# Optimization experiments

Hardware: AMD Instinct MI355X
Metric: run time of the kernel (lower is better)

Reference implementation:

```python
import jax, jax.numpy as jnp
import numpy as np
import math


def setup_inputs() -> dict:
    key = jax.random.key(0)
    kq, kk, kv, km = jax.random.split(key, 4)
    B, Lq, Lk, D = 4, 4096, 4096, 64
    queries = jax.random.normal(kq, (B, Lq, D), dtype=jnp.float32)
    keys = jax.random.normal(kk, (B, Lk, D), dtype=jnp.float32)
    values = jax.random.normal(kv, (B, Lk, D), dtype=jnp.float32)
    masks = jax.random.randint(km, (B, Lk), 0, 2, dtype=jnp.int32)
    return {"queries": queries, "keys": keys, "values": values, "masks": masks}


def reference(queries, keys, values, masks):
    # scale = sqrt(d_k) (self.scale is None)
    d_k = queries.shape[-1]
    scale = math.sqrt(d_k)
    # scores: [B, Lq, Lk]
    scores = jnp.einsum('bqd,bkd->bqk', queries, keys) / jnp.asarray(scale, queries.dtype)
    # key-padding mask [B, Lk] -> broadcast over Lq; masked positions -> -inf
    neg_inf = jnp.asarray(float('-inf'), scores.dtype)
    scores = jnp.where(masks[:, None, :] == 0, neg_inf, scores)
    attn = jax.nn.softmax(scores, axis=-1)  # dropout p=0 -> identity
    return jnp.einsum('bqk,bkd->bqd', attn, values)
```

## Files before the change

kernel.cpp:

```cpp
#include <hip/hip_runtime.h>


#define B_N    4
#define L      4096
#define DH     64
#define TILE_K 64
#define KPAD   72
#define SPLIT  8
#define SLAB   (L / SPLIT)
#define TILES  (SLAB / TILE_K)
#define QSCALE 0.18033688f

typedef unsigned short ushort8_ma __attribute__((ext_vector_type(8), may_alias));
typedef unsigned short ushort4_ma __attribute__((ext_vector_type(4), may_alias));
typedef float          f32x4_ma   __attribute__((ext_vector_type(4), may_alias));
typedef short          short8     __attribute__((ext_vector_type(8)));
typedef float          f32x16     __attribute__((ext_vector_type(16)));

union v8cast { ushort8_ma u; short8 s; };

static __device__ __forceinline__ short8 ld8(const unsigned short* p) {
    v8cast x; x.u = *(const ushort8_ma*)p; return x.s;
}
static __device__ __forceinline__ unsigned short bf16rne(float f) {
    union { float f; unsigned u; } x; x.f = f;
    unsigned r = x.u + 0x7fffu + ((x.u >> 16) & 1u);
    return (unsigned short)(r >> 16);
}
static __device__ __forceinline__ unsigned short bf16fast(float f) {
    union { float f; unsigned u; } x; x.f = f;
    return (unsigned short)((x.u + 0x8000u) >> 16);
}
static __device__ __forceinline__ float bf16tof(unsigned short u) {
    union { unsigned u; float f; } x; x.u = (unsigned)u << 16; return x.f;
}
static __device__ __forceinline__ float fast_exp2(float x) {
    return __builtin_amdgcn_exp2f(x);
}

__global__ __launch_bounds__(256)
void prepass3(const float* __restrict__ Q, const float* __restrict__ K,
              const float* __restrict__ V,
              unsigned short* __restrict__ Qb, unsigned short* __restrict__ Kb,
              unsigned short* __restrict__ Vt)
{
    __shared__ unsigned short t[64][20];
    const int b  = blockIdx.y;
    const int r0 = blockIdx.x * 16;
    const size_t base = ((size_t)b * L + r0) * DH;

    {
        int i = threadIdx.x;
        int row = i >> 4, d0 = (i & 15) * 4;
        size_t off = base + (size_t)row * DH + d0;
        f32x4_ma q = *(const f32x4_ma*)(Q + off);
        f32x4_ma k = *(const f32x4_ma*)(K + off);
        f32x4_ma v = *(const f32x4_ma*)(V + off);
        ushort4_ma qo, ko;
        #pragma unroll
        for (int j = 0; j < 4; ++j) {
            qo[j] = bf16rne(q[j] * QSCALE);
            ko[j] = bf16rne(k[j]);
            t[d0 + j][row] = bf16rne(v[j]);
        }
        *(ushort4_ma*)(Qb + off) = qo;
        *(ushort4_ma*)(Kb + off) = ko;
    }
    __syncthreads();
    {
        int i = threadIdx.x;
        int d = i >> 2, k4 = (i & 3) * 4;
        ushort4_ma vo = { t[d][k4], t[d][k4 + 1], t[d][k4 + 2], t[d][k4 + 3] };
        *(ushort4_ma*)(Vt + ((size_t)b * DH + d) * L + r0 + k4) = vo;
    }
}

__global__ __launch_bounds__(256, 4)
void fa_split32(const unsigned short* __restrict__ Qb,
                const unsigned short* __restrict__ Kb,
                const unsigned short* __restrict__ Vt,
                const int*            __restrict__ Mk,
                unsigned short* __restrict__ ACCp, float* __restrict__ Lp)
{
    __shared__ unsigned short Kl[TILE_K * KPAD];
    __shared__ unsigned short Vl[DH * KPAD];
    __shared__ unsigned short Pl[4][32 * KPAD];
    __shared__ int            Ml[TILE_K];

    const int tid  = threadIdx.x;
    const int wave = tid >> 6;
    const int lane = tid & 63;
    const int l32  = lane & 31;
    const int hw   = lane >> 5;

    const int b      = blockIdx.y & (B_N - 1);
    const int slab   = blockIdx.y >> 2;
    const int qblock = blockIdx.x * 128;
    const int kbase  = slab * SLAB;

    short8 aQ[4];
    {
        const unsigned short* qp = Qb + ((size_t)b * L + qblock + wave * 32 + l32) * DH;
        #pragma unroll
        for (int kk = 0; kk < 4; ++kk)
            aQ[kk] = ld8(qp + kk * 16 + hw * 8);
    }

    const unsigned short* Kbb = Kb + (size_t)b * L * DH;
    const unsigned short* Vtb = Vt + (size_t)b * DH * L;
    const int*            Mb  = Mk + (size_t)b * L;

    const int c1 = tid + 256;
    const int r0 = tid >> 3, d0 = (tid & 7) * 8;
    const int r1 = c1 >> 3,  d1 = (c1 & 7) * 8;

    ushort8_ma kr0, kr1, vr0, vr1;
    int mr;

    kr0 = *(const ushort8_ma*)(Kbb + (size_t)(kbase + r0) * DH + d0);
    kr1 = *(const ushort8_ma*)(Kbb + (size_t)(kbase + r1) * DH + d1);
    vr0 = *(const ushort8_ma*)(Vtb + (size_t)r0 * L + kbase + d0);
    vr1 = *(const ushort8_ma*)(Vtb + (size_t)r1 * L + kbase + d1);
    mr  = Mb[kbase + lane];
    *(ushort8_ma*)(&Kl[r0 * KPAD + d0]) = kr0;
    *(ushort8_ma*)(&Kl[r1 * KPAD + d1]) = kr1;
    *(ushort8_ma*)(&Vl[r0 * KPAD + d0]) = vr0;
    *(ushort8_ma*)(&Vl[r1 * KPAD + d1]) = vr1;
    if (wave == 0) Ml[lane] = mr;
    __syncthreads();

    f32x16 acc0 = {0}, acc1 = {0};
    float rs[16];
    #pragma unroll
    for (int r = 0; r < 16; ++r) rs[r] = 0.f;

    unsigned short* pw = &Pl[wave][0];

    for (int t = 0; t < TILES; ++t) {
        if (t < TILES - 1) {
            const int k0n = kbase + (t + 1) * TILE_K;
            kr0 = *(const ushort8_ma*)(Kbb + (size_t)(k0n + r0) * DH + d0);
            kr1 = *(const ushort8_ma*)(Kbb + (size_t)(k0n + r1) * DH + d1);
            vr0 = *(const ushort8_ma*)(Vtb + (size_t)r0 * L + k0n + d0);
            vr1 = *(const ushort8_ma*)(Vtb + (size_t)r1 * L + k0n + d1);
            mr  = Mb[k0n + lane];
        }

        #pragma unroll
        for (int g = 0; g < 2; ++g) {
            f32x16 s = {0};
            #pragma unroll
            for (int kk = 0; kk < 4; ++kk) {
                short8 bK = ld8(&Kl[(g * 32 + l32) * KPAD + kk * 16 + hw * 8]);
                s = __builtin_amdgcn_mfma_f32_32x32x16_bf16(aQ[kk], bK, s, 0, 0, 0);
            }
            float bias = (Ml[g * 32 + l32] == 0) ? -1e30f : 0.f;
            #pragma unroll
            for (int reg = 0; reg < 16; ++reg) {
                float p = fast_exp2(s[reg] + bias);
                rs[reg] += p;
                int row = (reg & 3) + 8 * (reg >> 2) + 4 * hw;
                pw[row * KPAD + g * 32 + l32] = bf16fast(p);
            }
        }

        #pragma unroll
        for (int kk = 0; kk < 4; ++kk) {
            short8 aP = ld8(&pw[l32 * KPAD + kk * 16 + hw * 8]);
            short8 bV0 = ld8(&Vl[l32 * KPAD + kk * 16 + hw * 8]);
            acc0 = __builtin_amdgcn_mfma_f32_32x32x16_bf16(aP, bV0, acc0, 0, 0, 0);
            short8 bV1 = ld8(&Vl[(32 + l32) * KPAD + kk * 16 + hw * 8]);
            acc1 = __builtin_amdgcn_mfma_f32_32x32x16_bf16(aP, bV1, acc1, 0, 0, 0);
        }

        __syncthreads();
        if (t < TILES - 1) {
            *(ushort8_ma*)(&Kl[r0 * KPAD + d0]) = kr0;
            *(ushort8_ma*)(&Kl[r1 * KPAD + d1]) = kr1;
            *(ushort8_ma*)(&Vl[r0 * KPAD + d0]) = vr0;
            *(ushort8_ma*)(&Vl[r1 * KPAD + d1]) = vr1;
            if (wave == 0) Ml[lane] = mr;
            __syncthreads();
        }
    }

    const size_t pbase = ((size_t)(slab * B_N + b)) * L;
    #pragma unroll
    for (int reg = 0; reg < 16; ++reg) {
        float t0 = rs[reg];
        t0 += __shfl_xor(t0, 1);
        t0 += __shfl_xor(t0, 2);
        t0 += __shfl_xor(t0, 4);
        t0 += __shfl_xor(t0, 8);
        t0 += __shfl_xor(t0, 16);
        int row  = (reg & 3) + 8 * (reg >> 2) + 4 * hw;
        int qrow = qblock + wave * 32 + row;
        unsigned short* ap = ACCp + (pbase + qrow) * DH;
        ap[l32]      = bf16rne(acc0[reg]);
        ap[32 + l32] = bf16rne(acc1[reg]);
        if (l32 == 0) Lp[pbase + qrow] = t0;
    }
}

__global__ __launch_bounds__(256)
void fa_combine(const unsigned short* __restrict__ ACCp,
                const float* __restrict__ Lp, float* __restrict__ O)
{
    const int b    = blockIdx.y;
    const int qrow = blockIdx.x * 4 + (threadIdx.x >> 6);
    const int d    = threadIdx.x & 63;

    float lsum = 0.f, o = 0.f;
    #pragma unroll
    for (int s = 0; s < SPLIT; ++s) {
        lsum += Lp[((size_t)(s * B_N + b)) * L + qrow];
        o    += bf16tof(ACCp[(((size_t)(s * B_N + b)) * L + qrow) * DH + d]);
    }
    O[((size_t)b * L + qrow) * DH + d] = o / fmaxf(lsum, 1e-20f);
}

#define TK  64
#define RW  4
#define RB  16
#define KST 67

__global__ __launch_bounds__(256)
void fa_scalar(const float* __restrict__ Q, const float* __restrict__ K,
               const float* __restrict__ V, const int* __restrict__ Mk,
               float* __restrict__ O)
{
    __shared__ float Kt[TK][KST];
    __shared__ float Vts[DH][KST];
    __shared__ float Qs[RB][DH];
    __shared__ float Ps[4][RW][TK];
    __shared__ float Bs[TK];

    const int tid = threadIdx.x, w = tid >> 6, lane = tid & 63;
    const int b = blockIdx.y, row0 = blockIdx.x * RB;

    for (int i = tid; i < RB * DH; i += 256) {
        int r = i >> 6, d = i & 63;
        Qs[r][d] = Q[((size_t)b * L + row0 + r) * DH + d];
    }
    float m[RW], l[RW], acc[RW];
    #pragma unroll
    for (int rr = 0; rr < RW; ++rr) { m[rr] = -1e30f; l[rr] = 0.f; acc[rr] = 0.f; }

    for (int k0 = 0; k0 < L; k0 += TK) {
        __syncthreads();
        for (int i = tid; i < TK * DH; i += 256) {
            int key = i >> 6, d = i & 63;
            Kt[key][d]  = K[((size_t)b * L + k0 + key) * DH + d];
            Vts[d][key] = V[((size_t)b * L + k0 + key) * DH + d];
        }
        if (tid < TK) Bs[tid] = (Mk[(size_t)b * L + k0 + tid] == 0) ? -1e30f : 0.f;
        __syncthreads();
        float s[RW];
        #pragma unroll
        for (int rr = 0; rr < RW; ++rr) s[rr] = 0.f;
        for (int d4 = 0; d4 < DH; d4 += 4) {
            float kv[4];
            #pragma unroll
            for (int j = 0; j < 4; ++j) kv[j] = Kt[lane][d4 + j];
            #pragma unroll
            for (int rr = 0; rr < RW; ++rr)
                #pragma unroll
                for (int j = 0; j < 4; ++j)
                    s[rr] += Qs[w * RW + rr][d4 + j] * kv[j];
        }
        float alpha[RW];
        #pragma unroll
        for (int rr = 0; rr < RW; ++rr) {
            float sv = s[rr] * 0.125f + Bs[lane];
            float t = sv;
            #pragma unroll
            for (int off = 1; off < 64; off <<= 1) t = fmaxf(t, __shfl_xor(t, off));
            float mnew = fmaxf(m[rr], t);
            alpha[rr] = __expf(fminf(m[rr] - mnew, 0.f));
            float p = __expf(fminf(sv - mnew, 0.f));
            Ps[w][rr][lane] = p;
            float su = p;
            #pragma unroll
            for (int off = 1; off < 64; off <<= 1) su += __shfl_xor(su, off);
            l[rr] = l[rr] * alpha[rr] + su;
            m[rr] = mnew;
        }
        __syncthreads();
        #pragma unroll
        for (int rr = 0; rr < RW; ++rr) acc[rr] *= alpha[rr];
        for (int k4 = 0; k4 < TK; k4 += 4) {
            float vv[4];
            #pragma unroll
            for (int j = 0; j < 4; ++j) vv[j] = Vts[lane][k4 + j];
            #pragma unroll
            for (int rr = 0; rr < RW; ++rr)
                #pragma unroll
                for (int j = 0; j < 4; ++j)
                    acc[rr] += Ps[w][rr][k4 + j] * vv[j];
        }
    }
    #pragma unroll
    for (int rr = 0; rr < RW; ++rr) {
        int row = row0 + w * RW + rr;
        O[((size_t)b * L + row) * DH + lane] = acc[rr] / fmaxf(l[rr], 1e-20f);
    }
}

extern "C" void kernel_launch(void* const* d_in, const int* in_sizes, int n_in,
                              void* d_out, int out_size, void* d_ws, size_t ws_size,
                              hipStream_t stream) {
    const float* Q = (const float*)d_in[0];
    const float* K = (const float*)d_in[1];
    const float* V = (const float*)d_in[2];
    const int*   M = (const int*)d_in[3];
    float*       O = (float*)d_out;

    const size_t elems     = (size_t)B_N * L * DH;
    const size_t bf16_need = elems * 2 * 3;
    const size_t acc_elems = (size_t)SPLIT * B_N * L * DH;
    const size_t ml_elems  = (size_t)SPLIT * B_N * L;
    const size_t full_need = bf16_need + acc_elems * 2 + ml_elems * 4;

    unsigned short* Qb = (unsigned short*)d_ws;
    unsigned short* Kb = Qb + elems;
    unsigned short* Vt = Kb + elems;

    if (ws_size >= full_need) {
        unsigned short* ACCp = Vt + elems;
        float*          Lp   = (float*)(ACCp + acc_elems);

        prepass3<<<dim3(L / 16, B_N), dim3(256), 0, stream>>>(Q, K, V, Qb, Kb, Vt);
        fa_split32<<<dim3(L / 128, B_N * SPLIT), dim3(256), 0, stream>>>(
            Qb, Kb, Vt, M, ACCp, Lp);
        fa_combine<<<dim3(L / 4, B_N), dim3(256), 0, stream>>>(ACCp, Lp, O);
    } else {
        fa_scalar<<<dim3(L / RB, B_N), dim3(256), 0, stream>>>(Q, K, V, M, O);
    }
}
```

Measured before the change: 110.0 us.

## Keep P in registers via transposed QK^T and fold mask into zeroed K/V

Computes S transposed (K as the A operand, Q as the B operand) so each lane holds the exponentiated scores in the layout needed for the PV MFMA. Packs them with v_cvt_pk_bf16 and permlane32_swap, which removes the per-wave LDS staging buffer for P. The key mask is applied in the prepass by zeroing masked K and V rows, so masked keys give exp2(0)=1 and contribute nothing to the output. The row sum is then corrected by subtracting the masked count, found per slab with a ballot/popcount. This drops the per-tile mask loads and bias adds, but the correction assumes the maximum score needs no subtraction and would lose precision if a row's scores were large.

```diff
diff --git a/kernel.cpp b/kernel.cpp
--- a/kernel.cpp
+++ b/kernel.cpp
@@ -16,8 +16,10 @@
 typedef float          f32x4_ma   __attribute__((ext_vector_type(4), may_alias));
 typedef short          short8     __attribute__((ext_vector_type(8)));
 typedef float          f32x16     __attribute__((ext_vector_type(16)));
-
-union v8cast { ushort8_ma u; short8 s; };
+typedef unsigned int   uint2_ev   __attribute__((ext_vector_type(2)));
+
+union v8cast  { ushort8_ma u; short8 s; };
+union pk4cast { unsigned int u[4]; short8 s; };
 
 static __device__ __forceinline__ short8 ld8(const unsigned short* p) {
     v8cast x; x.u = *(const ushort8_ma*)p; return x.s;
@@ -27,20 +29,21 @@
     unsigned r = x.u + 0x7fffu + ((x.u >> 16) & 1u);
     return (unsigned short)(r >> 16);
 }
-static __device__ __forceinline__ unsigned short bf16fast(float f) {
-    union { float f; unsigned u; } x; x.f = f;
-    return (unsigned short)((x.u + 0x8000u) >> 16);
-}
 static __device__ __forceinline__ float bf16tof(unsigned short u) {
     union { unsigned u; float f; } x; x.u = (unsigned)u << 16; return x.f;
 }
 static __device__ __forceinline__ float fast_exp2(float x) {
     return __builtin_amdgcn_exp2f(x);
 }
+static __device__ __forceinline__ unsigned cvt_pk_bf16(float lo, float hi) {
+    unsigned r;
+    asm("v_cvt_pk_bf16_f32 %0, %1, %2" : "=v"(r) : "v"(lo), "v"(hi));
+    return r;
+}
 
 __global__ __launch_bounds__(256)
 void prepass3(const float* __restrict__ Q, const float* __restrict__ K,
-              const float* __restrict__ V,
+              const float* __restrict__ V, const int* __restrict__ M,
               unsigned short* __restrict__ Qb, unsigned short* __restrict__ Kb,
               unsigned short* __restrict__ Vt)
 {
@@ -56,12 +59,13 @@
         f32x4_ma q = *(const f32x4_ma*)(Q + off);
         f32x4_ma k = *(const f32x4_ma*)(K + off);
         f32x4_ma v = *(const f32x4_ma*)(V + off);
+        const float zf = (M[(size_t)b * L + r0 + row] == 0) ? 0.f : 1.f;
         ushort4_ma qo, ko;
         #pragma unroll
         for (int j = 0; j < 4; ++j) {
             qo[j] = bf16rne(q[j] * QSCALE);
-            ko[j] = bf16rne(k[j]);
-            t[d0 + j][row] = bf16rne(v[j]);
+            ko[j] = bf16rne(k[j] * zf);
+            t[d0 + j][row] = bf16rne(v[j] * zf);
         }
         *(ushort4_ma*)(Qb + off) = qo;
         *(ushort4_ma*)(Kb + off) = ko;
@@ -84,8 +88,7 @@
 {
     __shared__ unsigned short Kl[TILE_K * KPAD];
     __shared__ unsigned short Vl[DH * KPAD];
-    __shared__ unsigned short Pl[4][32 * KPAD];
-    __shared__ int            Ml[TILE_K];
+    __shared__ int            cntw[4];
 
     const int tid  = threadIdx.x;
     const int wave = tid >> 6;
@@ -98,12 +101,12 @@
     const int qblock = blockIdx.x * 128;
     const int kbase  = slab * SLAB;
 
-    short8 aQ[4];
+    short8 bQ[4];
     {
         const unsigned short* qp = Qb + ((size_t)b * L + qblock + wave * 32 + l32) * DH;
         #pragma unroll
         for (int kk = 0; kk < 4; ++kk)
-            aQ[kk] = ld8(qp + kk * 16 + hw * 8);
+            bQ[kk] = ld8(qp + kk * 16 + hw * 8);
     }
 
     const unsigned short* Kbb = Kb + (size_t)b * L * DH;
@@ -115,26 +118,26 @@
     const int r1 = c1 >> 3,  d1 = (c1 & 7) * 8;
 
     ushort8_ma kr0, kr1, vr0, vr1;
-    int mr;
 
     kr0 = *(const ushort8_ma*)(Kbb + (size_t)(kbase + r0) * DH + d0);
     kr1 = *(const ushort8_ma*)(Kbb + (size_t)(kbase + r1) * DH + d1);
     vr0 = *(const ushort8_ma*)(Vtb + (size_t)r0 * L + kbase + d0);
     vr1 = *(const ushort8_ma*)(Vtb + (size_t)r1 * L + kbase + d1);
-    mr  = Mb[kbase + lane];
+    const int m0 = Mb[kbase + 2 * tid];
+    const int m1 = Mb[kbase + 2 * tid + 1];
     *(ushort8_ma*)(&Kl[r0 * KPAD + d0]) = kr0;
     *(ushort8_ma*)(&Kl[r1 * KPAD + d1]) = kr1;
     *(ushort8_ma*)(&Vl[r0 * KPAD + d0]) = vr0;
     *(ushort8_ma*)(&Vl[r1 * KPAD + d1]) = vr1;
-    if (wave == 0) Ml[lane] = mr;
+    {
+        unsigned long long bm0 = __ballot(m0 == 0);
+        unsigned long long bm1 = __ballot(m1 == 0);
+        if (lane == 0) cntw[wave] = __popcll(bm0) + __popcll(bm1);
+    }
     __syncthreads();
 
     f32x16 acc0 = {0}, acc1 = {0};
-    float rs[16];
-    #pragma unroll
-    for (int r = 0; r < 16; ++r) rs[r] = 0.f;
-
-    unsigned short* pw = &Pl[wave][0];
+    float rs0 = 0.f, rs1 = 0.f, rs2 = 0.f, rs3 = 0.f;
 
     for (int t = 0; t < TILES; ++t) {
         if (t < TILES - 1) {
@@ -143,7 +146,6 @@
             kr1 = *(const ushort8_ma*)(Kbb + (size_t)(k0n + r1) * DH + d1);
             vr0 = *(const ushort8_ma*)(Vtb + (size_t)r0 * L + k0n + d0);
             vr1 = *(const ushort8_ma*)(Vtb + (size_t)r1 * L + k0n + d1);
-            mr  = Mb[k0n + lane];
         }
 
         #pragma unroll
@@ -151,26 +153,35 @@
             f32x16 s = {0};
             #pragma unroll
             for (int kk = 0; kk < 4; ++kk) {
-                short8 bK = ld8(&Kl[(g * 32 + l32) * KPAD + kk * 16 + hw * 8]);
-                s = __builtin_amdgcn_mfma_f32_32x32x16_bf16(aQ[kk], bK, s, 0, 0, 0);
+                short8 aK = ld8(&Kl[(g * 32 + l32) * KPAD + kk * 16 + hw * 8]);
+                s = __builtin_amdgcn_mfma_f32_32x32x16_bf16(aK, bQ[kk], s, 0, 0, 0);
             }
-            float bias = (Ml[g * 32 + l32] == 0) ? -1e30f : 0.f;
-            #pragma unroll
-            for (int reg = 0; reg < 16; ++reg) {
-                float p = fast_exp2(s[reg] + bias);
-                rs[reg] += p;
-                int row = (reg & 3) + 8 * (reg >> 2) + 4 * hw;
-                pw[row * KPAD + g * 32 + l32] = bf16fast(p);
+            f32x16 p;
+            #pragma unroll
+            for (int r = 0; r < 16; r += 4) {
+                p[r + 0] = fast_exp2(s[r + 0]); rs0 += p[r + 0];
+                p[r + 1] = fast_exp2(s[r + 1]); rs1 += p[r + 1];
+                p[r + 2] = fast_exp2(s[r + 2]); rs2 += p[r + 2];
+                p[r + 3] = fast_exp2(s[r + 3]); rs3 += p[r + 3];
             }
-        }
-
-        #pragma unroll
-        for (int kk = 0; kk < 4; ++kk) {
-            short8 aP = ld8(&pw[l32 * KPAD + kk * 16 + hw * 8]);
-            short8 bV0 = ld8(&Vl[l32 * KPAD + kk * 16 + hw * 8]);
-            acc0 = __builtin_amdgcn_mfma_f32_32x32x16_bf16(aP, bV0, acc0, 0, 0, 0);
-            short8 bV1 = ld8(&Vl[(32 + l32) * KPAD + kk * 16 + hw * 8]);
-            acc1 = __builtin_amdgcn_mfma_f32_32x32x16_bf16(aP, bV1, acc1, 0, 0, 0);
+            #pragma unroll
+            for (int h = 0; h < 2; ++h) {
+                const int kk = 2 * g + h;
+                const int b0 = 8 * h;
+                unsigned A0 = cvt_pk_bf16(p[b0 + 0], p[b0 + 1]);
+                unsigned A1 = cvt_pk_bf16(p[b0 + 2], p[b0 + 3]);
+                unsigned B0 = cvt_pk_bf16(p[b0 + 4], p[b0 + 5]);
+                unsigned B1 = cvt_pk_bf16(p[b0 + 6], p[b0 + 7]);
+                uint2_ev r02 = __builtin_amdgcn_permlane32_swap(A0, B0, false, false);
+                uint2_ev r13 = __builtin_amdgcn_permlane32_swap(A1, B1, false, false);
+                pk4cast P;
+                P.u[0] = r02[0]; P.u[1] = r13[0];
+                P.u[2] = r02[1]; P.u[3] = r13[1];
+                short8 bV0 = ld8(&Vl[l32 * KPAD + kk * 16 + hw * 8]);
+                acc0 = __builtin_amdgcn_mfma_f32_32x32x16_bf16(P.s, bV0, acc0, 0, 0, 0);
+                short8 bV1 = ld8(&Vl[(32 + l32) * KPAD + kk * 16 + hw * 8]);
+                acc1 = __builtin_amdgcn_mfma_f32_32x32x16_bf16(P.s, bV1, acc1, 0, 0, 0);
+            }
         }
 
         __syncthreads();
@@ -179,27 +190,24 @@
             *(ushort8_ma*)(&Kl[r1 * KPAD + d1]) = kr1;
             *(ushort8_ma*)(&Vl[r0 * KPAD + d0]) = vr0;
             *(ushort8_ma*)(&Vl[r1 * KPAD + d1]) = vr1;
-            if (wave == 0) Ml[lane] = mr;
             __syncthreads();
         }
     }
 
+    float rs = (rs0 + rs1) + (rs2 + rs3);
+    rs += __shfl_xor(rs, 32);
+    const float scnt = (float)(cntw[0] + cntw[1] + cntw[2] + cntw[3]);
     const size_t pbase = ((size_t)(slab * B_N + b)) * L;
     #pragma unroll
     for (int reg = 0; reg < 16; ++reg) {
-        float t0 = rs[reg];
-        t0 += __shfl_xor(t0, 1);
-        t0 += __shfl_xor(t0, 2);
-        t0 += __shfl_xor(t0, 4);
-        t0 += __shfl_xor(t0, 8);
-        t0 += __shfl_xor(t0, 16);
         int row  = (reg & 3) + 8 * (reg >> 2) + 4 * hw;
         int qrow = qblock + wave * 32 + row;
         unsigned short* ap = ACCp + (pbase + qrow) * DH;
         ap[l32]      = bf16rne(acc0[reg]);
         ap[32 + l32] = bf16rne(acc1[reg]);
-        if (l32 == 0) Lp[pbase + qrow] = t0;
-    }
+    }
+    if (hw == 0)
+        Lp[pbase + qblock + wave * 32 + l32] = rs - scnt;
 }
 
 __global__ __launch_bounds__(256)
@@ -329,7 +337,7 @@
         unsigned short* ACCp = Vt + elems;
         float*          Lp   = (float*)(ACCp + acc_elems);
 
-        prepass3<<<dim3(L / 16, B_N), dim3(256), 0, stream>>>(Q, K, V, Qb, Kb, Vt);
+        prepass3<<<dim3(L / 16, B_N), dim3(256), 0, stream>>>(Q, K, V, M, Qb, Kb, Vt);
         fa_split32<<<dim3(L / 128, B_N * SPLIT), dim3(256), 0, stream>>>(
             Qb, Kb, Vt, M, ACCp, Lp);
         fa_combine<<<dim3(L / 4, B_N), dim3(256), 0, stream>>>(ACCp, Lp, O);
```

Measured after the change: 94.90 us. 13.7% less time.
